# Kernel tuning notes

Hardware: AMD Instinct MI355X
Metric: run time of the kernel (lower is better)

## Reference

```python
import jax, jax.numpy as jnp
import numpy as np

B, N, C = 4, 2048, 768
H = 12
D = C // H  # head_dim = 64


def setup_inputs() -> dict:
    key = jax.random.key(0)
    k1, k2, k3, k4, k5 = jax.random.split(key, 5)
    s = 0.02
    return {
        "x": jax.random.normal(k1, (B, N, C), dtype=jnp.float32),
        "qkv_w": jax.random.normal(k2, (3 * C, C), dtype=jnp.float32) * s,
        "qkv_b": jax.random.normal(k3, (3 * C,), dtype=jnp.float32) * s,
        "proj_w": jax.random.normal(k4, (C, C), dtype=jnp.float32) * s,
        "proj_b": jax.random.normal(k5, (C,), dtype=jnp.float32) * s,
    }


def reference(x, qkv_w, qkv_b, proj_w, proj_b):
    b, n, c = x.shape
    # qkv projection (torch Linear: x @ W.T + b) -> [B,N,3,H,D] -> [3,B,H,N,D]
    qkv = (x @ qkv_w.T + qkv_b).reshape(b, n, 3, H, D).transpose(2, 0, 3, 1, 4)
    q, k, v = qkv[0], qkv[1], qkv[2]
    scale = D ** (-0.5)
    attn = jnp.einsum("bhqd,bhkd->bhqk", q, k) * scale
    attn = jax.nn.softmax(attn, axis=-1)
    # dropout is identity in eval mode
    out = jnp.einsum("bhqk,bhkd->bhqd", attn, v)  # [B,H,N,D]
    out = out.transpose(0, 2, 1, 3).reshape(b, n, c)
    return out @ proj_w.T + proj_b
```

## Files before the change

kernel.cpp:

```cpp
#include <hip/hip_runtime.h>
#include <hip/hip_bf16.h>
#include <stdint.h>

typedef __bf16 bf16_t;
typedef __bf16 bf16x8 __attribute__((ext_vector_type(8)));
typedef float f32x4 __attribute__((ext_vector_type(4)));
typedef unsigned int u32x4 __attribute__((ext_vector_type(4)));

#define NB 4
#define NH 12
#define ND 64
#define NN 2048
#define NC 768

__device__ __forceinline__ void async_copy16(const bf16_t* g, bf16_t* l) {
    __builtin_amdgcn_global_load_lds((__attribute__((address_space(1))) void*)(void*)g,
                                     (__attribute__((address_space(3))) void*)l, 16, 0, 0);
}

__device__ __forceinline__ unsigned pack_bf2(float a, float b) {
    union { bf16_t e[2]; unsigned u; } t;
    t.e[0] = (bf16_t)a;
    t.e[1] = (bf16_t)b;
    return t.u;
}

__global__ void cast3_kernel(const float* __restrict__ s0, bf16_t* __restrict__ d0, int n0,
                             const float* __restrict__ s1, bf16_t* __restrict__ d1, int n1,
                             const float* __restrict__ s2, bf16_t* __restrict__ d2, int n2) {
    int i = blockIdx.x * blockDim.x + threadIdx.x;
    const float* s;
    bf16_t* d;
    int j;
    if (i < n0)           { s = s0; d = d0; j = i; }
    else if (i < n0 + n1) { s = s1; d = d1; j = i - n0; }
    else if (i < n0 + n1 + n2) { s = s2; d = d2; j = i - n0 - n1; }
    else return;
    float4 v = ((const float4*)s)[j];
    union { bf16_t e[4]; uint2 u; } t;
    t.e[0] = (bf16_t)v.x; t.e[1] = (bf16_t)v.y; t.e[2] = (bf16_t)v.z; t.e[3] = (bf16_t)v.w;
    ((uint2*)d)[j] = t.u;
}

__device__ __forceinline__ int vperm(int s) {
    return (s & 32) | (((s >> 2) & 3) << 3) | (((s >> 4) & 1) << 2) | (s & 3);
}


__launch_bounds__(256)
__global__ void qkv_gemm_kernel(const bf16_t* __restrict__ X, const bf16_t* __restrict__ W,
                                const float* __restrict__ bias,
                                bf16_t* __restrict__ Q, bf16_t* __restrict__ K, bf16_t* __restrict__ V)
{
    __shared__ __align__(16) bf16_t sA[128 * 64];
    __shared__ __align__(16) bf16_t sB[128 * 64];
    const int tid  = threadIdx.x;
    const int lane = tid & 63;
    const int w    = tid >> 6;
    const int wm   = w & 1, wn = w >> 1;
    const int m0   = blockIdx.x * 128;
    const int n0   = blockIdx.y * 128;
    const int lrow = lane & 15;
    const int quad = lane >> 4;
    const int arow = lane >> 3;
    const int gch  = (lane & 7) ^ arow;

    f32x4 zero = {0.f, 0.f, 0.f, 0.f};
    f32x4 acc[4][4];
#pragma unroll
    for (int i = 0; i < 4; ++i)
#pragma unroll
        for (int j = 0; j < 4; ++j) acc[i][j] = zero;

    for (int kt = 0; kt < NC; kt += 64) {
        __syncthreads();
        for (int c = w; c < 16; c += 4) {
            async_copy16(X + (size_t)(m0 + c * 8 + arow) * NC + kt + gch * 8, sA + c * 512);
            async_copy16(W + (size_t)(n0 + c * 8 + arow) * NC + kt + gch * 8, sB + c * 512);
        }
        __syncthreads();
#pragma unroll
        for (int hh = 0; hh < 2; ++hh) {
            bf16x8 af[4], bfr[4];
#pragma unroll
            for (int i = 0; i < 4; ++i) {
                int r = wm * 64 + i * 16 + lrow;
                af[i] = *(const bf16x8*)(sA + r * 64 + (((hh * 4 + quad) ^ (r & 7)) * 8));
            }
#pragma unroll
            for (int j = 0; j < 4; ++j) {
                int r = wn * 64 + j * 16 + lrow;
                bfr[j] = *(const bf16x8*)(sB + r * 64 + (((hh * 4 + quad) ^ (r & 7)) * 8));
            }
#pragma unroll
            for (int i = 0; i < 4; ++i)
#pragma unroll
                for (int j = 0; j < 4; ++j)
                    acc[i][j] = __builtin_amdgcn_mfma_f32_16x16x32_bf16(af[i], bfr[j], acc[i][j], 0, 0, 0);
        }
    }

    const int colbase = n0 + wn * 64;
    const int t3 = colbase / NC;
    const int h  = (colbase % NC) / ND;
    const float qscale = 0.125f * 1.44269504088896340736f;

#pragma unroll
    for (int j = 0; j < 4; ++j) {
        const int d  = j * 16 + lrow;
        const float bv = bias[colbase + d];
#pragma unroll
        for (int i = 0; i < 4; ++i) {
            const int rowg = m0 + wm * 64 + i * 16 + quad * 4;
            const int bb = rowg >> 11;
            const int nn = rowg & 2047;
            if (t3 == 2) {
                union { bf16_t e[4]; uint2 u; } pk;
#pragma unroll
                for (int p = 0; p < 4; ++p) pk.e[p] = (bf16_t)(acc[i][j][p] + bv);
                const int pos = (nn & ~63) | vperm(nn & 63);
                *(uint2*)(V + ((size_t)(bb * NH + h) * ND + d) * NN + pos) = pk.u;
            } else {
                bf16_t* outb = t3 ? K : Q;
#pragma unroll
                for (int p = 0; p < 4; ++p) {
                    float val = acc[i][j][p] + bv;
                    if (t3 == 0) val *= qscale;
                    outb[((size_t)(bb * NH + h) * NN + nn + p) * ND + d] = (bf16_t)val;
                }
            }
        }
    }
}

#define WAIT_BAR(N)                                              \
    asm volatile("s_waitcnt vmcnt(" #N ")" ::: "memory");        \
    __builtin_amdgcn_sched_barrier(0);                           \
    __builtin_amdgcn_s_barrier();                                \
    __builtin_amdgcn_sched_barrier(0);

#define STAGE(BUF)                                               \
    {                                                            \
        bf16_t* dK = sK[BUF] + w * 1024;                         \
        bf16_t* dV = sV[BUF] + w * 1024;                         \
        async_copy16(kp,          dK);                           \
        async_copy16(kp + 8 * ND, dK + 512);                     \
        async_copy16(vp,          dV);                           \
        async_copy16(vp + 8 * NN, dV + 512);                     \
        kp += (size_t)64 * ND; vp += 64;                         \
    }

#define ATTN_COMPUTE(CUR)                                                                            \
    {                                                                                                \
        const bf16_t* sKh = sK[CUR];                                                                 \
        const bf16_t* sVh = sV[CUR];                                                                 \
        f32x4 s[2][4];                                                                               \
        __builtin_amdgcn_s_setprio(1);                                                               \
        _Pragma("unroll")                                                                            \
        for (int blk = 0; blk < 4; ++blk) {                                                          \
            bf16x8 a0 = *(const bf16x8*)(sKh + off[blk][0]);                                         \
            bf16x8 a1 = *(const bf16x8*)(sKh + off[blk][1]);                                         \
            _Pragma("unroll")                                                                        \
            for (int qi = 0; qi < 2; ++qi) {                                                         \
                f32x4 z = zero;                                                                      \
                z = __builtin_amdgcn_mfma_f32_16x16x32_bf16(a0, qb[qi][0], z, 0, 0, 0);              \
                z = __builtin_amdgcn_mfma_f32_16x16x32_bf16(a1, qb[qi][1], z, 0, 0, 0);              \
                s[qi][blk] = z;                                                                      \
            }                                                                                        \
        }                                                                                            \
        __builtin_amdgcn_s_setprio(0);                                                               \
        bf16x8 pe[2][2];                                                                             \
        _Pragma("unroll")                                                                            \
        for (int qi = 0; qi < 2; ++qi) {                                                             \
            u32x4 pu0 = {0, 0, 0, 0}, pu1 = {0, 0, 0, 0};                                            \
            _Pragma("unroll")                                                                        \
            for (int blk = 0; blk < 4; ++blk) {                                                      \
                float e0 = __builtin_amdgcn_exp2f(s[qi][blk][0]);                                    \
                float e1 = __builtin_amdgcn_exp2f(s[qi][blk][1]);                                    \
                float e2 = __builtin_amdgcn_exp2f(s[qi][blk][2]);                                    \
                float e3 = __builtin_amdgcn_exp2f(s[qi][blk][3]);                                    \
                unsigned lo = pack_bf2(e0, e1), hi = pack_bf2(e2, e3);                               \
                if (blk == 0)      { pu0[0] = lo; pu0[1] = hi; }                                     \
                else if (blk == 1) { pu0[2] = lo; pu0[3] = hi; }                                     \
                else if (blk == 2) { pu1[0] = lo; pu1[1] = hi; }                                     \
                else               { pu1[2] = lo; pu1[3] = hi; }                                     \
            }                                                                                        \
            pe[qi][0] = __builtin_bit_cast(bf16x8, pu0);                                             \
            pe[qi][1] = __builtin_bit_cast(bf16x8, pu1);                                             \
        }                                                                                            \
        __builtin_amdgcn_s_setprio(1);                                                               \
        _Pragma("unroll")                                                                            \
        for (int qi = 0; qi < 2; ++qi) {                                                             \
            lacc[qi] = __builtin_amdgcn_mfma_f32_16x16x32_bf16(ones, pe[qi][0], lacc[qi], 0, 0, 0);  \
            lacc[qi] = __builtin_amdgcn_mfma_f32_16x16x32_bf16(ones, pe[qi][1], lacc[qi], 0, 0, 0);  \
        }                                                                                            \
        _Pragma("unroll")                                                                            \
        for (int db = 0; db < 4; ++db) {                                                             \
            bf16x8 v0 = *(const bf16x8*)(sVh + off[db][0]);                                          \
            bf16x8 v1 = *(const bf16x8*)(sVh + off[db][1]);                                          \
            _Pragma("unroll")                                                                        \
            for (int qi = 0; qi < 2; ++qi) {                                                         \
                o[qi][db] = __builtin_amdgcn_mfma_f32_16x16x32_bf16(v0, pe[qi][0], o[qi][db], 0, 0, 0); \
                o[qi][db] = __builtin_amdgcn_mfma_f32_16x16x32_bf16(v1, pe[qi][1], o[qi][db], 0, 0, 0); \
            }                                                                                        \
        }                                                                                            \
        __builtin_amdgcn_s_setprio(0);                                                               \
    }

__launch_bounds__(256, 3)
__global__ void attn_kernel(const bf16_t* __restrict__ Q, const bf16_t* __restrict__ K,
                            const bf16_t* __restrict__ Vt, bf16_t* __restrict__ O)
{
    __shared__ __align__(16) bf16_t sK[3][64 * 64];
    __shared__ __align__(16) bf16_t sV[3][64 * 64];
    bf16_t* sQ = sK[0];
    const int tid  = threadIdx.x;
    const int lane = tid & 63;
    const int w    = tid >> 6;
    const int qt   = blockIdx.x;
    const int h    = blockIdx.y;
    const int b    = blockIdx.z;
    const int lrow = lane & 15;
    const int quad = lane >> 4;
    const int arow = lane >> 3;
    const int gch  = (lane & 7) ^ arow;
    const size_t head_off = (size_t)(b * NH + h) * NN * ND;
    const bf16_t* qh = Q  + head_off;
    const bf16_t* kh = K  + head_off;
    const bf16_t* vh = Vt + head_off;

#pragma unroll
    for (int c = 0; c < 4; ++c)
        async_copy16(qh + (size_t)(qt * 128 + (w * 4 + c) * 8 + arow) * ND + gch * 8,
                     sQ + (w * 4 + c) * 512);
    __syncthreads();

    bf16x8 qb[2][2];
#pragma unroll
    for (int qi = 0; qi < 2; ++qi)
#pragma unroll
        for (int hh = 0; hh < 2; ++hh) {
            int r = w * 32 + qi * 16 + lrow;
            qb[qi][hh] = *(const bf16x8*)(sQ + r * 64 + (((hh * 4 + quad) ^ (r & 7)) * 8));
        }
    __syncthreads();

    bf16x8 ones;
#pragma unroll
    for (int p = 0; p < 8; ++p) ones[p] = (bf16_t)1.0f;

    int off[4][2];
#pragma unroll
    for (int blk = 0; blk < 4; ++blk) {
        int r = blk * 16 + lrow;
        off[blk][0] = r * 64 + ((quad ^ (r & 7)) * 8);
        off[blk][1] = r * 64 + (((4 + quad) ^ (r & 7)) * 8);
    }

    f32x4 zero = {0.f, 0.f, 0.f, 0.f};
    f32x4 o[2][4];
#pragma unroll
    for (int qi = 0; qi < 2; ++qi)
#pragma unroll
        for (int db = 0; db < 4; ++db) o[qi][db] = zero;
    f32x4 lacc[2] = {zero, zero};

    const bf16_t* kp = kh + (size_t)(w * 16 + arow) * ND + gch * 8;
    const bf16_t* vp = vh + (size_t)(w * 16 + arow) * NN + gch * 8;

    STAGE(0);
    STAGE(1);
    WAIT_BAR(4);

    int cur = 0;
    for (int it = 0; it < NN / 64 - 2; ++it) {
        int nxt = cur + 2; if (nxt >= 3) nxt -= 3;
        STAGE(nxt);
        ATTN_COMPUTE(cur);
        WAIT_BAR(4);
        cur = (cur + 1 == 3) ? 0 : cur + 1;
    }
    ATTN_COMPUTE(cur);
    WAIT_BAR(0);
    cur = (cur + 1 == 3) ? 0 : cur + 1;
    ATTN_COMPUTE(cur);

#pragma unroll
    for (int qi = 0; qi < 2; ++qi) {
        const float rl = 1.0f / lacc[qi][0];
        const int n = qt * 128 + w * 32 + qi * 16 + lrow;
        const size_t rowoff = ((size_t)(b * NN + n)) * NC + h * ND;
#pragma unroll
        for (int db = 0; db < 4; ++db) {
            union { bf16_t e[4]; uint2 u; } pk;
#pragma unroll
            for (int p = 0; p < 4; ++p) pk.e[p] = (bf16_t)(o[qi][db][p] * rl);
            *(uint2*)(O + rowoff + db * 16 + quad * 4) = pk.u;
        }
    }
}

__launch_bounds__(256)
__global__ void proj_gemm_kernel(const bf16_t* __restrict__ A, const bf16_t* __restrict__ W,
                                 const float* __restrict__ bias, float* __restrict__ out)
{
    __shared__ __align__(16) bf16_t sA[128 * 64];
    __shared__ __align__(16) bf16_t sB[128 * 64];
    const int tid  = threadIdx.x;
    const int lane = tid & 63;
    const int w    = tid >> 6;
    const int wm   = w & 1, wn = w >> 1;
    const int m0   = blockIdx.x * 128;
    const int n0   = blockIdx.y * 128;
    const int lrow = lane & 15;
    const int quad = lane >> 4;
    const int arow = lane >> 3;
    const int gch  = (lane & 7) ^ arow;

    f32x4 zero = {0.f, 0.f, 0.f, 0.f};
    f32x4 acc[4][4];
#pragma unroll
    for (int i = 0; i < 4; ++i)
#pragma unroll
        for (int j = 0; j < 4; ++j) acc[i][j] = zero;

    for (int kt = 0; kt < NC; kt += 64) {
        __syncthreads();
        for (int c = w; c < 16; c += 4) {
            async_copy16(A + (size_t)(m0 + c * 8 + arow) * NC + kt + gch * 8, sA + c * 512);
            async_copy16(W + (size_t)(n0 + c * 8 + arow) * NC + kt + gch * 8, sB + c * 512);
        }
        __syncthreads();
#pragma unroll
        for (int hh = 0; hh < 2; ++hh) {
            bf16x8 af[4], bfr[4];
#pragma unroll
            for (int i = 0; i < 4; ++i) {
                int r = wm * 64 + i * 16 + lrow;
                af[i] = *(const bf16x8*)(sA + r * 64 + (((hh * 4 + quad) ^ (r & 7)) * 8));
            }
#pragma unroll
            for (int j = 0; j < 4; ++j) {
                int r = wn * 64 + j * 16 + lrow;
                bfr[j] = *(const bf16x8*)(sB + r * 64 + (((hh * 4 + quad) ^ (r & 7)) * 8));
            }
#pragma unroll
            for (int i = 0; i < 4; ++i)
#pragma unroll
                for (int j = 0; j < 4; ++j)
                    acc[i][j] = __builtin_amdgcn_mfma_f32_16x16x32_bf16(af[i], bfr[j], acc[i][j], 0, 0, 0);
        }
    }

#pragma unroll
    for (int j = 0; j < 4; ++j) {
        const int colg = n0 + wn * 64 + j * 16 + lrow;
        const float bv = bias[colg];
#pragma unroll
        for (int i = 0; i < 4; ++i) {
            const int rowg = m0 + wm * 64 + i * 16 + quad * 4;
#pragma unroll
            for (int p = 0; p < 4; ++p)
                out[(size_t)(rowg + p) * NC + colg] = acc[i][j][p] + bv;
        }
    }
}

extern "C" void kernel_launch(void* const* d_in, const int* in_sizes, int n_in,
                              void* d_out, int out_size, void* d_ws, size_t ws_size,
                              hipStream_t stream) {
    const float* x      = (const float*)d_in[0];
    const float* qkv_w  = (const float*)d_in[1];
    const float* qkv_b  = (const float*)d_in[2];
    const float* proj_w = (const float*)d_in[3];
    const float* proj_b = (const float*)d_in[4];
    float* out = (float*)d_out;

    char* ws = (char*)d_ws;
    bf16_t* xb    = (bf16_t*)ws; ws += (size_t)8192 * 768 * 2;
    bf16_t* wqkv  = (bf16_t*)ws; ws += (size_t)2304 * 768 * 2;
    bf16_t* wproj = (bf16_t*)ws; ws += (size_t)768 * 768 * 2;
    bf16_t* qb    = (bf16_t*)ws; ws += (size_t)NB * NH * NN * ND * 2;
    bf16_t* kb    = (bf16_t*)ws; ws += (size_t)NB * NH * NN * ND * 2;
    bf16_t* vb    = (bf16_t*)ws; ws += (size_t)NB * NH * NN * ND * 2;
    bf16_t* ab    = (bf16_t*)ws; ws += (size_t)8192 * 768 * 2;

    const int c0 = 8192 * 768 / 4, c1 = 2304 * 768 / 4, c2 = 768 * 768 / 4;
    cast3_kernel<<<(c0 + c1 + c2 + 255) / 256, 256, 0, stream>>>(x, xb, c0, qkv_w, wqkv, c1, proj_w, wproj, c2);

    qkv_gemm_kernel<<<dim3(8192 / 128, 2304 / 128), 256, 0, stream>>>(xb, wqkv, qkv_b, qb, kb, vb);
    attn_kernel<<<dim3(NN / 128, NH, NB), 256, 0, stream>>>(qb, kb, vb, ab);
    proj_gemm_kernel<<<dim3(8192 / 128, 768 / 128), 256, 0, stream>>>(ab, wproj, proj_b, out);
}
```

Baseline: 212.0 us.

## Split attention tile across 8 waves, one 16-row query slice each

The attention kernel moves from 4 waves of 32 query rows to 8 waves of 16 query rows per 128-row tile, using 512 threads per block. Each wave now holds half the accumulators and Q fragments, and the K/V staging is spread across twice as many threads, each issuing one async copy per buffer. The aim is more waves in flight per CU to hide latency. In exchange, each K/V fragment read from LDS feeds only one query sub-tile instead of two, so LDS traffic per MFMA doubles.

```diff
diff --git a/kernel.cpp b/kernel.cpp
--- a/kernel.cpp
+++ b/kernel.cpp
@@ -141,12 +141,8 @@
 
 #define STAGE(BUF)                                               \
     {                                                            \
-        bf16_t* dK = sK[BUF] + w * 1024;                         \
-        bf16_t* dV = sV[BUF] + w * 1024;                         \
-        async_copy16(kp,          dK);                           \
-        async_copy16(kp + 8 * ND, dK + 512);                     \
-        async_copy16(vp,          dV);                           \
-        async_copy16(vp + 8 * NN, dV + 512);                     \
+        async_copy16(kp, sK[BUF] + w * 512);                     \
+        async_copy16(vp, sV[BUF] + w * 512);                     \
         kp += (size_t)64 * ND; vp += 64;                         \
     }
 
@@ -154,60 +150,47 @@
     {                                                                                                \
         const bf16_t* sKh = sK[CUR];                                                                 \
         const bf16_t* sVh = sV[CUR];                                                                 \
-        f32x4 s[2][4];                                                                               \
+        f32x4 s[4];                                                                                  \
         __builtin_amdgcn_s_setprio(1);                                                               \
         _Pragma("unroll")                                                                            \
         for (int blk = 0; blk < 4; ++blk) {                                                          \
             bf16x8 a0 = *(const bf16x8*)(sKh + off[blk][0]);                                         \
             bf16x8 a1 = *(const bf16x8*)(sKh + off[blk][1]);                                         \
-            _Pragma("unroll")                                                                        \
-            for (int qi = 0; qi < 2; ++qi) {                                                         \
-                f32x4 z = zero;                                                                      \
-                z = __builtin_amdgcn_mfma_f32_16x16x32_bf16(a0, qb[qi][0], z, 0, 0, 0);              \
-                z = __builtin_amdgcn_mfma_f32_16x16x32_bf16(a1, qb[qi][1], z, 0, 0, 0);              \
-                s[qi][blk] = z;                                                                      \
-            }                                                                                        \
+            f32x4 z = zero;                                                                          \
+            z = __builtin_amdgcn_mfma_f32_16x16x32_bf16(a0, qb0, z, 0, 0, 0);                        \
+            z = __builtin_amdgcn_mfma_f32_16x16x32_bf16(a1, qb1, z, 0, 0, 0);                        \
+            s[blk] = z;                                                                              \
         }                                                                                            \
         __builtin_amdgcn_s_setprio(0);                                                               \
-        bf16x8 pe[2][2];                                                                             \
+        u32x4 pu0 = {0, 0, 0, 0}, pu1 = {0, 0, 0, 0};                                                \
         _Pragma("unroll")                                                                            \
-        for (int qi = 0; qi < 2; ++qi) {                                                             \
-            u32x4 pu0 = {0, 0, 0, 0}, pu1 = {0, 0, 0, 0};                                            \
-            _Pragma("unroll")                                                                        \
-            for (int blk = 0; blk < 4; ++blk) {                                                      \
-                float e0 = __builtin_amdgcn_exp2f(s[qi][blk][0]);                                    \
-                float e1 = __builtin_amdgcn_exp2f(s[qi][blk][1]);                                    \
-                float e2 = __builtin_amdgcn_exp2f(s[qi][blk][2]);                                    \
-                float e3 = __builtin_amdgcn_exp2f(s[qi][blk][3]);                                    \
-                unsigned lo = pack_bf2(e0, e1), hi = pack_bf2(e2, e3);                               \
-                if (blk == 0)      { pu0[0] = lo; pu0[1] = hi; }                                     \
-                else if (blk == 1) { pu0[2] = lo; pu0[3] = hi; }                                     \
-                else if (blk == 2) { pu1[0] = lo; pu1[1] = hi; }                                     \
-                else               { pu1[2] = lo; pu1[3] = hi; }                                     \
-            }                                                                                        \
-            pe[qi][0] = __builtin_bit_cast(bf16x8, pu0);                                             \
-            pe[qi][1] = __builtin_bit_cast(bf16x8, pu1);                                             \
+        for (int blk = 0; blk < 4; ++blk) {                                                          \
+            float e0 = __builtin_amdgcn_exp2f(s[blk][0]);                                            \
+            float e1 = __builtin_amdgcn_exp2f(s[blk][1]);                                            \
+            float e2 = __builtin_amdgcn_exp2f(s[blk][2]);                                            \
+            float e3 = __builtin_amdgcn_exp2f(s[blk][3]);                                            \
+            unsigned lo = pack_bf2(e0, e1), hi = pack_bf2(e2, e3);                                   \
+            if (blk == 0)      { pu0[0] = lo; pu0[1] = hi; }                                         \
+            else if (blk == 1) { pu0[2] = lo; pu0[3] = hi; }                                         \
+            else if (blk == 2) { pu1[0] = lo; pu1[1] = hi; }                                         \
+            else               { pu1[2] = lo; pu1[3] = hi; }                                         \
         }                                                                                            \
+        bf16x8 pe0 = __builtin_bit_cast(bf16x8, pu0);                                                \
+        bf16x8 pe1 = __builtin_bit_cast(bf16x8, pu1);                                                \
         __builtin_amdgcn_s_setprio(1);                                                               \
-        _Pragma("unroll")                                                                            \
-        for (int qi = 0; qi < 2; ++qi) {                                                             \
-            lacc[qi] = __builtin_amdgcn_mfma_f32_16x16x32_bf16(ones, pe[qi][0], lacc[qi], 0, 0, 0);  \
-            lacc[qi] = __builtin_amdgcn_mfma_f32_16x16x32_bf16(ones, pe[qi][1], lacc[qi], 0, 0, 0);  \
-        }                                                                                            \
+        lacc = __builtin_amdgcn_mfma_f32_16x16x32_bf16(ones, pe0, lacc, 0, 0, 0);                    \
+        lacc = __builtin_amdgcn_mfma_f32_16x16x32_bf16(ones, pe1, lacc, 0, 0, 0);                    \
         _Pragma("unroll")                                                                            \
         for (int db = 0; db < 4; ++db) {                                                             \
             bf16x8 v0 = *(const bf16x8*)(sVh + off[db][0]);                                          \
             bf16x8 v1 = *(const bf16x8*)(sVh + off[db][1]);                                          \
-            _Pragma("unroll")                                                                        \
-            for (int qi = 0; qi < 2; ++qi) {                                                         \
-                o[qi][db] = __builtin_amdgcn_mfma_f32_16x16x32_bf16(v0, pe[qi][0], o[qi][db], 0, 0, 0); \
-                o[qi][db] = __builtin_amdgcn_mfma_f32_16x16x32_bf16(v1, pe[qi][1], o[qi][db], 0, 0, 0); \
-            }                                                                                        \
+            o[db] = __builtin_amdgcn_mfma_f32_16x16x32_bf16(v0, pe0, o[db], 0, 0, 0);                \
+            o[db] = __builtin_amdgcn_mfma_f32_16x16x32_bf16(v1, pe1, o[db], 0, 0, 0);                \
         }                                                                                            \
         __builtin_amdgcn_s_setprio(0);                                                               \
     }
 
-__launch_bounds__(256, 3)
+__launch_bounds__(512, 6)
 __global__ void attn_kernel(const bf16_t* __restrict__ Q, const bf16_t* __restrict__ K,
                             const bf16_t* __restrict__ Vt, bf16_t* __restrict__ O)
 {
@@ -230,19 +213,17 @@
     const bf16_t* vh = Vt + head_off;
 
 #pragma unroll
-    for (int c = 0; c < 4; ++c)
-        async_copy16(qh + (size_t)(qt * 128 + (w * 4 + c) * 8 + arow) * ND + gch * 8,
-                     sQ + (w * 4 + c) * 512);
+    for (int c = 0; c < 2; ++c)
+        async_copy16(qh + (size_t)(qt * 128 + (w * 2 + c) * 8 + arow) * ND + gch * 8,
+                     sQ + (w * 2 + c) * 512);
     __syncthreads();
 
-    bf16x8 qb[2][2];
-#pragma unroll
-    for (int qi = 0; qi < 2; ++qi)
-#pragma unroll
-        for (int hh = 0; hh < 2; ++hh) {
-            int r = w * 32 + qi * 16 + lrow;
-            qb[qi][hh] = *(const bf16x8*)(sQ + r * 64 + (((hh * 4 + quad) ^ (r & 7)) * 8));
-        }
+    bf16x8 qb0, qb1;
+    {
+        int r = w * 16 + lrow;
+        qb0 = *(const bf16x8*)(sQ + r * 64 + (((0 * 4 + quad) ^ (r & 7)) * 8));
+        qb1 = *(const bf16x8*)(sQ + r * 64 + (((1 * 4 + quad) ^ (r & 7)) * 8));
+    }
     __syncthreads();
 
     bf16x8 ones;
@@ -258,26 +239,24 @@
     }
 
     f32x4 zero = {0.f, 0.f, 0.f, 0.f};
-    f32x4 o[2][4];
-#pragma unroll
-    for (int qi = 0; qi < 2; ++qi)
-#pragma unroll
-        for (int db = 0; db < 4; ++db) o[qi][db] = zero;
-    f32x4 lacc[2] = {zero, zero};
-
-    const bf16_t* kp = kh + (size_t)(w * 16 + arow) * ND + gch * 8;
-    const bf16_t* vp = vh + (size_t)(w * 16 + arow) * NN + gch * 8;
+    f32x4 o[4];
+#pragma unroll
+    for (int db = 0; db < 4; ++db) o[db] = zero;
+    f32x4 lacc = zero;
+
+    const bf16_t* kp = kh + (size_t)(w * 8 + arow) * ND + gch * 8;
+    const bf16_t* vp = vh + (size_t)(w * 8 + arow) * NN + gch * 8;
 
     STAGE(0);
     STAGE(1);
-    WAIT_BAR(4);
+    WAIT_BAR(2);
 
     int cur = 0;
     for (int it = 0; it < NN / 64 - 2; ++it) {
         int nxt = cur + 2; if (nxt >= 3) nxt -= 3;
         STAGE(nxt);
         ATTN_COMPUTE(cur);
-        WAIT_BAR(4);
+        WAIT_BAR(2);
         cur = (cur + 1 == 3) ? 0 : cur + 1;
     }
     ATTN_COMPUTE(cur);
@@ -285,16 +264,15 @@
     cur = (cur + 1 == 3) ? 0 : cur + 1;
     ATTN_COMPUTE(cur);
 
-#pragma unroll
-    for (int qi = 0; qi < 2; ++qi) {
-        const float rl = 1.0f / lacc[qi][0];
-        const int n = qt * 128 + w * 32 + qi * 16 + lrow;
+    {
+        const float rl = 1.0f / lacc[0];
+        const int n = qt * 128 + w * 16 + lrow;
         const size_t rowoff = ((size_t)(b * NN + n)) * NC + h * ND;
 #pragma unroll
         for (int db = 0; db < 4; ++db) {
             union { bf16_t e[4]; uint2 u; } pk;
 #pragma unroll
-            for (int p = 0; p < 4; ++p) pk.e[p] = (bf16_t)(o[qi][db][p] * rl);
+            for (int p = 0; p < 4; ++p) pk.e[p] = (bf16_t)(o[db][p] * rl);
             *(uint2*)(O + rowoff + db * 16 + quad * 4) = pk.u;
         }
     }
@@ -389,6 +367,6 @@
     cast3_kernel<<<(c0 + c1 + c2 + 255) / 256, 256, 0, stream>>>(x, xb, c0, qkv_w, wqkv, c1, proj_w, wproj, c2);
 
     qkv_gemm_kernel<<<dim3(8192 / 128, 2304 / 128), 256, 0, stream>>>(xb, wqkv, qkv_b, qb, kb, vb);
-    attn_kernel<<<dim3(NN / 128, NH, NB), 256, 0, stream>>>(qb, kb, vb, ab);
+    attn_kernel<<<dim3(NN / 128, NH, NB), 512, 0, stream>>>(qb, kb, vb, ab);
     proj_gemm_kernel<<<dim3(8192 / 128, 768 / 128), 256, 0, stream>>>(ab, wproj, proj_b, out);
 }
```

Result: slower. 217.3 us (+2.5%).

## Switch attention kernel to 32x32x16 MFMA tiles with cross-lane P shuffle

Applied to the files above, without the earlier changes.

Rewrites the attention inner loop to use 32x32x16 bf16 MFMA instead of 16x16x32. It processes the 64-key tile in two 32-key halves and rearranges the exponentiated scores into the B-operand layout with an xor-32 lane shuffle. Q fragments are now loaded directly from global memory instead of staged through LDS, and the V-transpose permutation in the QKV epilogue is dropped to match the new read pattern. The larger MFMA shape aims for higher matrix throughput per instruction and fewer LDS reads. In exchange it adds shuffle work and larger accumulator register pressure at 3 blocks per CU.

```diff
diff --git a/kernel.cpp b/kernel.cpp
--- a/kernel.cpp
+++ b/kernel.cpp
@@ -5,6 +5,7 @@
 typedef __bf16 bf16_t;
 typedef __bf16 bf16x8 __attribute__((ext_vector_type(8)));
 typedef float f32x4 __attribute__((ext_vector_type(4)));
+typedef float f32x16 __attribute__((ext_vector_type(16)));
 typedef unsigned int u32x4 __attribute__((ext_vector_type(4)));
 
 #define NB 4
@@ -40,10 +41,6 @@
     union { bf16_t e[4]; uint2 u; } t;
     t.e[0] = (bf16_t)v.x; t.e[1] = (bf16_t)v.y; t.e[2] = (bf16_t)v.z; t.e[3] = (bf16_t)v.w;
     ((uint2*)d)[j] = t.u;
-}
-
-__device__ __forceinline__ int vperm(int s) {
-    return (s & 32) | (((s >> 2) & 3) << 3) | (((s >> 4) & 1) << 2) | (s & 3);
 }
 
 
@@ -118,8 +115,7 @@
                 union { bf16_t e[4]; uint2 u; } pk;
 #pragma unroll
                 for (int p = 0; p < 4; ++p) pk.e[p] = (bf16_t)(acc[i][j][p] + bv);
-                const int pos = (nn & ~63) | vperm(nn & 63);
-                *(uint2*)(V + ((size_t)(bb * NH + h) * ND + d) * NN + pos) = pk.u;
+                *(uint2*)(V + ((size_t)(bb * NH + h) * ND + d) * NN + nn) = pk.u;
             } else {
                 bf16_t* outb = t3 ? K : Q;
 #pragma unroll
@@ -150,61 +146,51 @@
         kp += (size_t)64 * ND; vp += 64;                         \
     }
 
-#define ATTN_COMPUTE(CUR)                                                                            \
-    {                                                                                                \
-        const bf16_t* sKh = sK[CUR];                                                                 \
-        const bf16_t* sVh = sV[CUR];                                                                 \
-        f32x4 s[2][4];                                                                               \
-        __builtin_amdgcn_s_setprio(1);                                                               \
-        _Pragma("unroll")                                                                            \
-        for (int blk = 0; blk < 4; ++blk) {                                                          \
-            bf16x8 a0 = *(const bf16x8*)(sKh + off[blk][0]);                                         \
-            bf16x8 a1 = *(const bf16x8*)(sKh + off[blk][1]);                                         \
-            _Pragma("unroll")                                                                        \
-            for (int qi = 0; qi < 2; ++qi) {                                                         \
-                f32x4 z = zero;                                                                      \
-                z = __builtin_amdgcn_mfma_f32_16x16x32_bf16(a0, qb[qi][0], z, 0, 0, 0);              \
-                z = __builtin_amdgcn_mfma_f32_16x16x32_bf16(a1, qb[qi][1], z, 0, 0, 0);              \
-                s[qi][blk] = z;                                                                      \
-            }                                                                                        \
-        }                                                                                            \
-        __builtin_amdgcn_s_setprio(0);                                                               \
-        bf16x8 pe[2][2];                                                                             \
-        _Pragma("unroll")                                                                            \
-        for (int qi = 0; qi < 2; ++qi) {                                                             \
-            u32x4 pu0 = {0, 0, 0, 0}, pu1 = {0, 0, 0, 0};                                            \
-            _Pragma("unroll")                                                                        \
-            for (int blk = 0; blk < 4; ++blk) {                                                      \
-                float e0 = __builtin_amdgcn_exp2f(s[qi][blk][0]);                                    \
-                float e1 = __builtin_amdgcn_exp2f(s[qi][blk][1]);                                    \
-                float e2 = __builtin_amdgcn_exp2f(s[qi][blk][2]);                                    \
-                float e3 = __builtin_amdgcn_exp2f(s[qi][blk][3]);                                    \
-                unsigned lo = pack_bf2(e0, e1), hi = pack_bf2(e2, e3);                               \
-                if (blk == 0)      { pu0[0] = lo; pu0[1] = hi; }                                     \
-                else if (blk == 1) { pu0[2] = lo; pu0[3] = hi; }                                     \
-                else if (blk == 2) { pu1[0] = lo; pu1[1] = hi; }                                     \
-                else               { pu1[2] = lo; pu1[3] = hi; }                                     \
-            }                                                                                        \
-            pe[qi][0] = __builtin_bit_cast(bf16x8, pu0);                                             \
-            pe[qi][1] = __builtin_bit_cast(bf16x8, pu1);                                             \
-        }                                                                                            \
-        __builtin_amdgcn_s_setprio(1);                                                               \
-        _Pragma("unroll")                                                                            \
-        for (int qi = 0; qi < 2; ++qi) {                                                             \
-            lacc[qi] = __builtin_amdgcn_mfma_f32_16x16x32_bf16(ones, pe[qi][0], lacc[qi], 0, 0, 0);  \
-            lacc[qi] = __builtin_amdgcn_mfma_f32_16x16x32_bf16(ones, pe[qi][1], lacc[qi], 0, 0, 0);  \
-        }                                                                                            \
-        _Pragma("unroll")                                                                            \
-        for (int db = 0; db < 4; ++db) {                                                             \
-            bf16x8 v0 = *(const bf16x8*)(sVh + off[db][0]);                                          \
-            bf16x8 v1 = *(const bf16x8*)(sVh + off[db][1]);                                          \
-            _Pragma("unroll")                                                                        \
-            for (int qi = 0; qi < 2; ++qi) {                                                         \
-                o[qi][db] = __builtin_amdgcn_mfma_f32_16x16x32_bf16(v0, pe[qi][0], o[qi][db], 0, 0, 0); \
-                o[qi][db] = __builtin_amdgcn_mfma_f32_16x16x32_bf16(v1, pe[qi][1], o[qi][db], 0, 0, 0); \
-            }                                                                                        \
-        }                                                                                            \
-        __builtin_amdgcn_s_setprio(0);                                                               \
+#define ATTN_COMPUTE(CUR)                                                                        \
+    {                                                                                            \
+        const bf16_t* sKh = sK[CUR];                                                             \
+        const bf16_t* sVh = sV[CUR];                                                             \
+        _Pragma("unroll")                                                                        \
+        for (int kb = 0; kb < 2; ++kb) {                                                         \
+            f32x16 sc = zero16;                                                                  \
+            __builtin_amdgcn_s_setprio(1);                                                       \
+            _Pragma("unroll")                                                                    \
+            for (int ds = 0; ds < 4; ++ds) {                                                     \
+                bf16x8 a = *(const bf16x8*)(sKh + (kb * 32 + r32) * 64 +                         \
+                                            (((ds * 2 + hi) ^ (r32 & 7)) * 8));                  \
+                sc = __builtin_amdgcn_mfma_f32_32x32x16_bf16(a, qb[ds], sc, 0, 0, 0);            \
+            }                                                                                    \
+            __builtin_amdgcn_s_setprio(0);                                                       \
+            unsigned c[8], cx[8];                                                                \
+            _Pragma("unroll")                                                                    \
+            for (int t = 0; t < 8; ++t)                                                          \
+                c[t] = pack_bf2(__builtin_amdgcn_exp2f(sc[2 * t]),                               \
+                                __builtin_amdgcn_exp2f(sc[2 * t + 1]));                          \
+            _Pragma("unroll")                                                                    \
+            for (int t = 0; t < 8; ++t) cx[t] = (unsigned)__shfl_xor((int)c[t], 32);             \
+            bf16x8 pe[2];                                                                        \
+            _Pragma("unroll")                                                                    \
+            for (int s16 = 0; s16 < 2; ++s16) {                                                  \
+                u32x4 wv;                                                                        \
+                wv[0] = hi ? cx[s16 * 4 + 2] : c[s16 * 4 + 0];                                   \
+                wv[1] = hi ? cx[s16 * 4 + 3] : c[s16 * 4 + 1];                                   \
+                wv[2] = hi ? c[s16 * 4 + 2]  : cx[s16 * 4 + 0];                                  \
+                wv[3] = hi ? c[s16 * 4 + 3]  : cx[s16 * 4 + 1];                                  \
+                pe[s16] = __builtin_bit_cast(bf16x8, wv);                                        \
+            }                                                                                    \
+            __builtin_amdgcn_s_setprio(1);                                                       \
+            lacc = __builtin_amdgcn_mfma_f32_32x32x16_bf16(ones, pe[0], lacc, 0, 0, 0);          \
+            lacc = __builtin_amdgcn_mfma_f32_32x32x16_bf16(ones, pe[1], lacc, 0, 0, 0);          \
+            _Pragma("unroll")                                                                    \
+            for (int db = 0; db < 2; ++db)                                                       \
+                _Pragma("unroll")                                                                \
+                for (int s16 = 0; s16 < 2; ++s16) {                                              \
+                    bf16x8 v = *(const bf16x8*)(sVh + (db * 32 + r32) * 64 +                     \
+                                                ((((kb * 2 + s16) * 2 + hi) ^ (r32 & 7)) * 8));  \
+                    o[db] = __builtin_amdgcn_mfma_f32_32x32x16_bf16(v, pe[s16], o[db], 0, 0, 0); \
+                }                                                                                \
+            __builtin_amdgcn_s_setprio(0);                                                       \
+        }                                                                                        \
     }
 
 __launch_bounds__(256, 3)
@@ -213,15 +199,14 @@
 {
     __shared__ __align__(16) bf16_t sK[3][64 * 64];
     __shared__ __align__(16) bf16_t sV[3][64 * 64];
-    bf16_t* sQ = sK[0];
     const int tid  = threadIdx.x;
     const int lane = tid & 63;
     const int w    = tid >> 6;
     const int qt   = blockIdx.x;
     const int h    = blockIdx.y;
     const int b    = blockIdx.z;
-    const int lrow = lane & 15;
-    const int quad = lane >> 4;
+    const int r32  = lane & 31;
+    const int hi   = lane >> 5;
     const int arow = lane >> 3;
     const int gch  = (lane & 7) ^ arow;
     const size_t head_off = (size_t)(b * NH + h) * NN * ND;
@@ -229,41 +214,20 @@
     const bf16_t* kh = K  + head_off;
     const bf16_t* vh = Vt + head_off;
 
-#pragma unroll
-    for (int c = 0; c < 4; ++c)
-        async_copy16(qh + (size_t)(qt * 128 + (w * 4 + c) * 8 + arow) * ND + gch * 8,
-                     sQ + (w * 4 + c) * 512);
-    __syncthreads();
-
-    bf16x8 qb[2][2];
-#pragma unroll
-    for (int qi = 0; qi < 2; ++qi)
-#pragma unroll
-        for (int hh = 0; hh < 2; ++hh) {
-            int r = w * 32 + qi * 16 + lrow;
-            qb[qi][hh] = *(const bf16x8*)(sQ + r * 64 + (((hh * 4 + quad) ^ (r & 7)) * 8));
-        }
-    __syncthreads();
+    bf16x8 qb[4];
+#pragma unroll
+    for (int ds = 0; ds < 4; ++ds)
+        qb[ds] = *(const bf16x8*)(qh + (size_t)(qt * 128 + w * 32 + r32) * ND + ds * 16 + hi * 8);
 
     bf16x8 ones;
 #pragma unroll
     for (int p = 0; p < 8; ++p) ones[p] = (bf16_t)1.0f;
 
-    int off[4][2];
-#pragma unroll
-    for (int blk = 0; blk < 4; ++blk) {
-        int r = blk * 16 + lrow;
-        off[blk][0] = r * 64 + ((quad ^ (r & 7)) * 8);
-        off[blk][1] = r * 64 + (((4 + quad) ^ (r & 7)) * 8);
-    }
-
-    f32x4 zero = {0.f, 0.f, 0.f, 0.f};
-    f32x4 o[2][4];
-#pragma unroll
-    for (int qi = 0; qi < 2; ++qi)
-#pragma unroll
-        for (int db = 0; db < 4; ++db) o[qi][db] = zero;
-    f32x4 lacc[2] = {zero, zero};
+    f32x16 zero16 = {0.f, 0.f, 0.f, 0.f, 0.f, 0.f, 0.f, 0.f,
+                     0.f, 0.f, 0.f, 0.f, 0.f, 0.f, 0.f, 0.f};
+    f32x16 o[2];
+    o[0] = zero16; o[1] = zero16;
+    f32x16 lacc = zero16;
 
     const bf16_t* kp = kh + (size_t)(w * 16 + arow) * ND + gch * 8;
     const bf16_t* vp = vh + (size_t)(w * 16 + arow) * NN + gch * 8;
@@ -285,18 +249,19 @@
     cur = (cur + 1 == 3) ? 0 : cur + 1;
     ATTN_COMPUTE(cur);
 
-#pragma unroll
-    for (int qi = 0; qi < 2; ++qi) {
-        const float rl = 1.0f / lacc[qi][0];
-        const int n = qt * 128 + w * 32 + qi * 16 + lrow;
+    {
+        const float rl = 1.0f / lacc[0];
+        const int n = qt * 128 + w * 32 + r32;
         const size_t rowoff = ((size_t)(b * NN + n)) * NC + h * ND;
 #pragma unroll
-        for (int db = 0; db < 4; ++db) {
-            union { bf16_t e[4]; uint2 u; } pk;
-#pragma unroll
-            for (int p = 0; p < 4; ++p) pk.e[p] = (bf16_t)(o[qi][db][p] * rl);
-            *(uint2*)(O + rowoff + db * 16 + quad * 4) = pk.u;
-        }
+        for (int db = 0; db < 2; ++db)
+#pragma unroll
+            for (int t = 0; t < 4; ++t) {
+                union { bf16_t e[4]; uint2 u; } pk;
+#pragma unroll
+                for (int p = 0; p < 4; ++p) pk.e[p] = (bf16_t)(o[db][t * 4 + p] * rl);
+                *(uint2*)(O + rowoff + db * 32 + 8 * t + 4 * hi) = pk.u;
+            }
     }
 }
 
```

Result: slower. 220.1 us (+3.8%).
